# Performance work log

Measured on AMD Instinct MI355X. Metric: run time of the kernel, lower is better.

Reference implementation:

```python
import math
import jax, jax.numpy as jnp
import numpy as np

B, L, D, H = 4, 4096, 1024, 16
DK = D // H


def setup_inputs() -> dict:
    key = jax.random.key(0)
    ks = jax.random.split(key, 11)
    s = 0.02
    return {
        "queries": jax.random.normal(ks[0], (B, L, D), jnp.float32),
        "keys": jax.random.normal(ks[1], (B, L, D), jnp.float32),
        "values": jax.random.normal(ks[2], (B, L, D), jnp.float32),
        "Wq": jax.random.normal(ks[3], (D, D), jnp.float32) * s,
        "bq": jnp.zeros((D,), jnp.float32),
        "Wk": jax.random.normal(ks[4], (D, D), jnp.float32) * s,
        "bk": jnp.zeros((D,), jnp.float32),
        "Wv": jax.random.normal(ks[5], (D, D), jnp.float32) * s,
        "bv": jnp.zeros((D,), jnp.float32),
        "Wo": jax.random.normal(ks[6], (D, D), jnp.float32) * s,
        "bo": jnp.zeros((D,), jnp.float32),
    }


def reference(queries, keys, values, Wq, bq, Wk, bk, Wv, bv, Wo, bo):
    # projections + split heads: (B, H, L, DK)
    q = (queries @ Wq + bq).reshape(B, L, H, DK).transpose(0, 2, 1, 3)
    k = (keys @ Wk + bk).reshape(B, L, H, DK).transpose(0, 2, 1, 3)
    v = (values @ Wv + bv).reshape(B, L, H, DK).transpose(0, 2, 1, 3)

    # per-head mean over channel dim -> (B, H, L)
    qm = q.mean(axis=-1)
    km = k.mean(axis=-1)

    # FFT-based autocorrelation: corr (B, H, L)
    qf = jnp.fft.rfft(qm, axis=-1)
    kf = jnp.fft.rfft(km, axis=-1)
    corr = jnp.fft.irfft(qf * jnp.conj(kf), n=L, axis=-1)

    top_k = max(1, int(math.log(L)))  # top_k=None path -> 8 for L=4096
    w, delays = jax.lax.top_k(corr, top_k)          # (B, H, K)
    w = jax.nn.softmax(w, axis=-1)

    # torch.roll(x, shift=d): out[i] = x[(i - d) mod L]
    pos = jnp.arange(L)
    out = jnp.zeros_like(v)
    for kk in range(top_k):
        idx = (pos[None, None, :] - delays[:, :, kk, None]) % L  # (B, H, L)
        rolled = jnp.take_along_axis(v, idx[..., None], axis=2)  # (B, H, L, DK)
        out = out + w[:, :, kk, None, None] * rolled

    # merge heads (matches per-head concat order) and output projection
    out = out.transpose(0, 2, 1, 3).reshape(B, L, D)
    return out @ Wo + bo
```

## Files before the change

kernel.cpp:

```cpp
#include <hip/hip_runtime.h>
#include <hip/hip_bf16.h>
#include <cstdint>

#define BB 4
#define LL 4096
#define DD 1024
#define HH 16
#define DKH 64
#define MROWS 16384
#define KTOP 8
#define RPB 16

typedef float f32x4 __attribute__((ext_vector_type(4)));
typedef _Float16 f16;
typedef _Float16 f16x4 __attribute__((ext_vector_type(4)));
typedef _Float16 f16x8 __attribute__((ext_vector_type(8)));

__device__ __forceinline__ void gll16(const void* g, void* l) {
    __builtin_amdgcn_global_load_lds(
        (const __attribute__((address_space(1))) void*)g,
        (__attribute__((address_space(3))) void*)l, 16, 0, 0);
}

__global__ void k_colmeans(const float* __restrict__ Wq, const float* __restrict__ bq,
                           const float* __restrict__ Wk, const float* __restrict__ bk,
                           float* __restrict__ Wqm_t, float* __restrict__ Wkm_t,
                           float* __restrict__ bqm, float* __restrict__ bkm) {
    int t = blockIdx.x * blockDim.x + threadIdx.x;
    int which = t >> 14;
    int idx = t & 16383;
    int d = idx >> 4;
    int h = idx & 15;
    const float* W = which ? Wk : Wq;
    const float* p = W + d * DD + h * DKH;
    float s = 0.f;
    #pragma unroll
    for (int c = 0; c < DKH; ++c) s += p[c];
    (which ? Wkm_t : Wqm_t)[h * DD + d] = s * (1.0f / DKH);
    if (d == 0) {
        const float* bb = which ? bk : bq;
        float sb = 0.f;
        for (int c = 0; c < DKH; ++c) sb += bb[h * DKH + c];
        (which ? bkm : bqm)[h] = sb * (1.0f / DKH);
    }
}

__global__ void k_transpose_cvt(const float* __restrict__ in, f16* __restrict__ out) {
    __shared__ float tile[32][33];
    int k0 = blockIdx.x * 32;
    int n0 = blockIdx.y * 32;
    int tx = threadIdx.x, ty = threadIdx.y;
    #pragma unroll
    for (int j = 0; j < 32; j += 8)
        tile[ty + j][tx] = in[(k0 + ty + j) * DD + n0 + tx];
    __syncthreads();
    #pragma unroll
    for (int j = 0; j < 32; j += 8)
        out[(n0 + ty + j) * DD + k0 + tx] = (f16)tile[tx][ty + j];
}

__global__ void k_cvt_f16(const float* __restrict__ in, f16* __restrict__ out) {
    int i = blockIdx.x * blockDim.x + threadIdx.x;
    f32x4 v = ((const f32x4*)in)[i];
    f16x4 o;
    o[0] = (f16)v.x; o[1] = (f16)v.y; o[2] = (f16)v.z; o[3] = (f16)v.w;
    ((f16x4*)out)[i] = o;
}

__global__ __launch_bounds__(256, 4) void k_means(const float* __restrict__ q, const float* __restrict__ k,
                        const float* __restrict__ Wqm_t, const float* __restrict__ Wkm_t,
                        const float* __restrict__ bqm, const float* __restrict__ bkm,
                        float* __restrict__ qm, float* __restrict__ km) {
    __shared__ float lred[RPB * 64];
    int isK = blockIdx.x & 1;
    int rb  = blockIdx.x >> 1;
    const float* src = isK ? k : q;
    const float* W   = isK ? Wkm_t : Wqm_t;
    const float* bm  = isK ? bkm : bqm;
    float* dst = isK ? km : qm;
    int t = threadIdx.x;
    int wavei = t >> 6, lane = t & 63;
    int c = wavei * 256 + lane * 4;
    f32x4 wr[16];
    #pragma unroll
    for (int h = 0; h < 16; ++h) wr[h] = *(const f32x4*)(W + h * DD + c);
    const float* rbase = src + (size_t)rb * RPB * DD + c;
    #pragma unroll 2
    for (int r = 0; r < RPB; ++r) {
        f32x4 rv = *(const f32x4*)(rbase + r * DD);
        float v[16];
        #pragma unroll
        for (int h = 0; h < 16; ++h)
            v[h] = rv.x * wr[h].x + rv.y * wr[h].y + rv.z * wr[h].z + rv.w * wr[h].w;
        float u[8];
        #pragma unroll
        for (int i = 0; i < 8; ++i) {
            float keep = (lane & 1) ? v[2*i+1] : v[2*i];
            float send = (lane & 1) ? v[2*i]   : v[2*i+1];
            u[i] = keep + __shfl_xor(send, 1);
        }
        float w2[4];
        #pragma unroll
        for (int i = 0; i < 4; ++i) {
            float keep = (lane & 2) ? u[2*i+1] : u[2*i];
            float send = (lane & 2) ? u[2*i]   : u[2*i+1];
            w2[i] = keep + __shfl_xor(send, 2);
        }
        float y[2];
        #pragma unroll
        for (int i = 0; i < 2; ++i) {
            float keep = (lane & 4) ? w2[2*i+1] : w2[2*i];
            float send = (lane & 4) ? w2[2*i]   : w2[2*i+1];
            y[i] = keep + __shfl_xor(send, 4);
        }
        {
            float keep = (lane & 8) ? y[1] : y[0];
            float send = (lane & 8) ? y[0] : y[1];
            float z = keep + __shfl_xor(send, 8);
            z += __shfl_xor(z, 16);
            z += __shfl_xor(z, 32);
            if (lane < 16) lred[r * 64 + wavei * 16 + lane] = z;
        }
    }
    __syncthreads();
    int rr = t >> 4, h = t & 15;
    float s = lred[rr * 64 + h] + lred[rr * 64 + 16 + h]
            + lred[rr * 64 + 32 + h] + lred[rr * 64 + 48 + h] + bm[h];
    int row = rb * RPB + rr;
    int b = row >> 12, l = row & 4095;
    dst[((size_t)((b << 4) + h) << 12) + l] = s;
}

__global__ __launch_bounds__(1024) void k_corr(const float* __restrict__ qm,
                                               const float* __restrict__ km,
                                               float* __restrict__ corr) {
    __shared__ float sq[LL];
    __shared__ float sk[LL];
    __shared__ f32x4 red[1024];
    int bh = blockIdx.x >> 2;
    int lag0 = (blockIdx.x & 3) * 1024;
    const f32x4* qg = (const f32x4*)(qm + bh * LL);
    const f32x4* kg = (const f32x4*)(km + bh * LL);
    f32x4* sq4 = (f32x4*)sq;
    f32x4* sk4 = (f32x4*)sk;
    int t = threadIdx.x;
    for (int i = t; i < LL / 4; i += 1024) { sq4[i] = qg[i]; sk4[i] = kg[i]; }
    __syncthreads();
    int lt = t & 255;
    int ms = t >> 8;
    int d0 = lag0 + lt * 4;
    int m0 = ms * 1024;
    float a0 = 0, a1 = 0, a2 = 0, a3 = 0;
    f32x4 wv = sq4[((m0 + d0) & 4095) >> 2];
    float w0 = wv.x, w1 = wv.y, w2 = wv.z, w3 = wv.w;
    #pragma unroll 4
    for (int m = m0; m < m0 + 1024; m += 4) {
        f32x4 nx = sq4[((m + 4 + d0) & 4095) >> 2];
        f32x4 kv = sk4[m >> 2];
        a0 += kv.x * w0;  a1 += kv.x * w1;  a2 += kv.x * w2;  a3 += kv.x * w3;
        a0 += kv.y * w1;  a1 += kv.y * w2;  a2 += kv.y * w3;  a3 += kv.y * nx.x;
        a0 += kv.z * w2;  a1 += kv.z * w3;  a2 += kv.z * nx.x; a3 += kv.z * nx.y;
        a0 += kv.w * w3;  a1 += kv.w * nx.x; a2 += kv.w * nx.y; a3 += kv.w * nx.z;
        w0 = nx.x; w1 = nx.y; w2 = nx.z; w3 = nx.w;
    }
    f32x4 p; p.x = a0; p.y = a1; p.z = a2; p.w = a3;
    red[t] = p;
    __syncthreads();
    if (t < 256) {
        f32x4 s0 = red[t], s1 = red[256 + t], s2 = red[512 + t], s3 = red[768 + t];
        f32x4 s;
        s.x = s0.x + s1.x + s2.x + s3.x;
        s.y = s0.y + s1.y + s2.y + s3.y;
        s.z = s0.z + s1.z + s2.z + s3.z;
        s.w = s0.w + s1.w + s2.w + s3.w;
        *(f32x4*)(corr + bh * LL + lag0 + t * 4) = s;
    }
}

__global__ __launch_bounds__(256) void k_topk(const float* __restrict__ corr,
                                              float* __restrict__ wts, int* __restrict__ dls) {
    __shared__ float sc[LL];
    __shared__ float rv[4]; __shared__ int ri[4];
    __shared__ float topv[KTOP]; __shared__ int topi[KTOP];
    int bh = blockIdx.x;
    for (int i = threadIdx.x; i < LL; i += 256) sc[i] = corr[bh * LL + i];
    for (int kk = 0; kk < KTOP; ++kk) {
        __syncthreads();
        float bv = -1e30f; int bi = 0;
        for (int i = threadIdx.x; i < LL; i += 256) {
            float v = sc[i];
            if (v > bv) { bv = v; bi = i; }
        }
        #pragma unroll
        for (int off = 32; off; off >>= 1) {
            float ov = __shfl_down(bv, off);
            int oi = __shfl_down(bi, off);
            if (ov > bv || (ov == bv && oi < bi)) { bv = ov; bi = oi; }
        }
        int wid = threadIdx.x >> 6;
        if ((threadIdx.x & 63) == 0) { rv[wid] = bv; ri[wid] = bi; }
        __syncthreads();
        if (threadIdx.x == 0) {
            for (int w = 1; w < 4; ++w)
                if (rv[w] > bv || (rv[w] == bv && ri[w] < bi)) { bv = rv[w]; bi = ri[w]; }
            topv[kk] = bv; topi[kk] = bi;
            sc[bi] = -1e30f;
        }
    }
    __syncthreads();
    if (threadIdx.x == 0) {
        float mx = topv[0], s = 0.f, e[KTOP];
        #pragma unroll
        for (int kk = 0; kk < KTOP; ++kk) { e[kk] = __expf(topv[kk] - mx); s += e[kk]; }
        float inv = 1.0f / s;
        #pragma unroll
        for (int kk = 0; kk < KTOP; ++kk) {
            wts[bh * KTOP + kk] = e[kk] * inv;
            dls[bh * KTOP + kk] = topi[kk];
        }
    }
}

#define BM 128
#define BN 128
#define BKK 32
template <int MODE>
__global__ __launch_bounds__(256) void k_gemm_bt(const f16* __restrict__ A,
                                                 const f16* __restrict__ BT,
                                                 const float* __restrict__ bias,
                                                 void* __restrict__ Cout) {
    __shared__ f16 As[BM * BKK];
    __shared__ f16 Bs[BN * BKK];
    const int K = DD;
    int n0 = blockIdx.x * BN;
    int m0 = blockIdx.y * BM;
    int tid = threadIdx.x;
    int lane = tid & 63;
    int wave = tid >> 6;
    int wm = wave & 1, wn = wave >> 1;

    int row0 = tid >> 2;
    int slot = tid & 3;
    int kc0 = slot ^ ((row0 >> 1) & 3);
    int row1 = row0 + 64;
    int kc1 = slot ^ ((row1 >> 1) & 3);
    const f16* gA0 = A + (size_t)(m0 + row0) * K + kc0 * 8;
    const f16* gA1 = A + (size_t)(m0 + row1) * K + kc1 * 8;
    const f16* gB0 = BT + (size_t)(n0 + row0) * K + kc0 * 8;
    const f16* gB1 = BT + (size_t)(n0 + row1) * K + kc1 * 8;
    char* ldsA0 = (char*)As + wave * 1024;
    char* ldsA1 = (char*)As + 4096 + wave * 1024;
    char* ldsB0 = (char*)Bs + wave * 1024;
    char* ldsB1 = (char*)Bs + 4096 + wave * 1024;

    int fr = lane & 15;
    int quad = lane >> 4;
    int a_off[4], b_off[4];
    #pragma unroll
    for (int i = 0; i < 4; ++i) {
        int ra = wm * 64 + i * 16 + fr;
        a_off[i] = (ra * 4 + (quad ^ ((ra >> 1) & 3))) * 8;
        int rb = wn * 64 + i * 16 + fr;
        b_off[i] = (rb * 4 + (quad ^ ((rb >> 1) & 3))) * 8;
    }

    f32x4 acc[4][4] = {};
    for (int kt = 0; kt < K; kt += BKK) {
        __syncthreads();
        gll16(gA0, ldsA0);
        gll16(gA1, ldsA1);
        gll16(gB0, ldsB0);
        gll16(gB1, ldsB1);
        gA0 += BKK; gA1 += BKK; gB0 += BKK; gB1 += BKK;
        __syncthreads();
        f16x8 af[4], bf[4];
        #pragma unroll
        for (int i = 0; i < 4; ++i) af[i] = *(const f16x8*)(As + a_off[i]);
        #pragma unroll
        for (int i = 0; i < 4; ++i) bf[i] = *(const f16x8*)(Bs + b_off[i]);
        #pragma unroll
        for (int im = 0; im < 4; ++im)
            #pragma unroll
            for (int in = 0; in < 4; ++in)
                acc[im][in] = __builtin_amdgcn_mfma_f32_16x16x32_f16(af[im], bf[in], acc[im][in], 0, 0, 0);
    }

    #pragma unroll
    for (int in = 0; in < 4; ++in) {
        int col = n0 + wn * 64 + in * 16 + fr;
        float bb = bias[col];
        #pragma unroll
        for (int im = 0; im < 4; ++im) {
            int rowb = m0 + wm * 64 + im * 16 + quad * 4;
            #pragma unroll
            for (int r = 0; r < 4; ++r) {
                float val = acc[im][in][r] + bb;
                if (MODE == 0) {
                    int rr = rowb + r;
                    int b = rr >> 12, l = rr & 4095, h = col >> 6, c = col & 63;
                    ((f16*)Cout)[((size_t)(((b << 4) + h) << 12) + l) * 64 + c] = (f16)val;
                } else {
                    ((float*)Cout)[(size_t)(rowb + r) * DD + col] = val;
                }
            }
        }
    }
}

__global__ __launch_bounds__(256) void k_roll(const f16* __restrict__ V,
                                              const float* __restrict__ wts,
                                              const int* __restrict__ dls,
                                              f16* __restrict__ out) {
    int t = blockIdx.x * 256 + threadIdx.x;
    int cc = t & 7;
    int l = (t >> 3) & 4095;
    int bh = t >> 15;
    const f16* vb = V + ((size_t)bh << 18);
    float a[8] = {};
    #pragma unroll
    for (int kk = 0; kk < KTOP; ++kk) {
        float w = wts[bh * KTOP + kk];
        int d = dls[bh * KTOP + kk];
        int src = (l - d) & 4095;
        f16x8 vv = *(const f16x8*)(vb + (src << 6) + (cc << 3));
        #pragma unroll
        for (int j = 0; j < 8; ++j) a[j] += w * (float)vv[j];
    }
    f16* o = out + ((size_t)((bh >> 4) << 12) + l) * 1024 + ((bh & 15) << 6) + (cc << 3);
    f16x8 ov;
    #pragma unroll
    for (int j = 0; j < 8; ++j) ov[j] = (f16)a[j];
    *(f16x8*)o = ov;
}

extern "C" void kernel_launch(void* const* d_in, const int* in_sizes, int n_in,
                              void* d_out, int out_size, void* d_ws, size_t ws_size,
                              hipStream_t stream) {
    const float* queries = (const float*)d_in[0];
    const float* keys    = (const float*)d_in[1];
    const float* values  = (const float*)d_in[2];
    const float* Wq = (const float*)d_in[3];
    const float* bq = (const float*)d_in[4];
    const float* Wk = (const float*)d_in[5];
    const float* bk = (const float*)d_in[6];
    const float* Wv = (const float*)d_in[7];
    const float* bv = (const float*)d_in[8];
    const float* Wo = (const float*)d_in[9];
    const float* bo = (const float*)d_in[10];

    char* ws = (char*)d_ws;
    size_t off = 0;
    auto alloc = [&](size_t bytes) -> char* {
        char* p = ws + off;
        off += (bytes + 255) & ~(size_t)255;
        return p;
    };
    f16*   values_f16 = (f16*)alloc((size_t)MROWS * DD * 2);
    f16*   Vbuf       = (f16*)alloc((size_t)MROWS * DD * 2);
    f16*   WvT        = (f16*)alloc((size_t)DD * DD * 2);
    f16*   WoT        = (f16*)alloc((size_t)DD * DD * 2);
    float* Wqm_t      = (float*)alloc(HH * DD * 4);
    float* Wkm_t      = (float*)alloc(HH * DD * 4);
    float* bqm        = (float*)alloc(HH * 4);
    float* bkm        = (float*)alloc(HH * 4);
    float* qm         = (float*)alloc((size_t)BB * HH * LL * 4);
    float* km         = (float*)alloc((size_t)BB * HH * LL * 4);
    float* corr       = (float*)alloc((size_t)BB * HH * LL * 4);
    float* wts        = (float*)alloc(BB * HH * KTOP * 4);
    int*   dls        = (int*)alloc(BB * HH * KTOP * 4);
    f16*   out_f16    = values_f16;

    k_colmeans<<<128, 256, 0, stream>>>(Wq, bq, Wk, bk, Wqm_t, Wkm_t, bqm, bkm);
    k_transpose_cvt<<<dim3(32, 32), dim3(32, 8), 0, stream>>>(Wv, WvT);
    k_transpose_cvt<<<dim3(32, 32), dim3(32, 8), 0, stream>>>(Wo, WoT);
    k_cvt_f16<<<16384, 256, 0, stream>>>(values, values_f16);
    k_means<<<2048, 256, 0, stream>>>(queries, keys, Wqm_t, Wkm_t, bqm, bkm, qm, km);
    k_corr<<<256, 1024, 0, stream>>>(qm, km, corr);
    k_topk<<<64, 256, 0, stream>>>(corr, wts, dls);
    k_gemm_bt<0><<<dim3(DD / BN, MROWS / BM), 256, 0, stream>>>(values_f16, WvT, bv, Vbuf);
    k_roll<<<8192, 256, 0, stream>>>(Vbuf, wts, dls, out_f16);
    k_gemm_bt<1><<<dim3(DD / BN, MROWS / BM), 256, 0, stream>>>(out_f16, WoT, bo, d_out);
}
```

Measured before the change: 443.8 us.

## Use DPP reductions in means, drop LDS key copy in corr, swap GEMM grid order

In k_means, most cross-lane shuffles become DPP row operations, the next row is prefetched, and the final reduction moves partly into LDS with a larger, padded buffer. In k_corr, the key vector is no longer staged in LDS; it is read from global memory with a wave-uniform index so it can become a scalar/broadcast load. The GEMM grid is transposed so consecutive blocks walk along M rather than N, which changes which operand tiles are shared in L2. Together these aim to cut shuffle cost, LDS footprint and cache misses, at the risk of extra global traffic in k_corr and a different cache access pattern in the GEMMs.

```diff
diff --git a/kernel.cpp b/kernel.cpp
--- a/kernel.cpp
+++ b/kernel.cpp
@@ -20,6 +20,12 @@
     __builtin_amdgcn_global_load_lds(
         (const __attribute__((address_space(1))) void*)g,
         (__attribute__((address_space(3))) void*)l, 16, 0, 0);
+}
+
+template <int CTRL>
+__device__ __forceinline__ float dppf(float x) {
+    return __builtin_bit_cast(float,
+        __builtin_amdgcn_update_dpp(0, __builtin_bit_cast(int, x), CTRL, 0xF, 0xF, true));
 }
 
 __global__ void k_colmeans(const float* __restrict__ Wq, const float* __restrict__ bq,
@@ -71,7 +77,7 @@
                         const float* __restrict__ Wqm_t, const float* __restrict__ Wkm_t,
                         const float* __restrict__ bqm, const float* __restrict__ bkm,
                         float* __restrict__ qm, float* __restrict__ km) {
-    __shared__ float lred[RPB * 64];
+    __shared__ float lred[RPB * 264];
     int isK = blockIdx.x & 1;
     int rb  = blockIdx.x >> 1;
     const float* src = isK ? k : q;
@@ -84,10 +90,14 @@
     f32x4 wr[16];
     #pragma unroll
     for (int h = 0; h < 16; ++h) wr[h] = *(const f32x4*)(W + h * DD + c);
+    #pragma unroll
+    for (int h = 0; h < 16; ++h) asm volatile("" : "+v"(wr[h]));
     const float* rbase = src + (size_t)rb * RPB * DD + c;
-    #pragma unroll 2
+    f32x4 rv = *(const f32x4*)rbase;
+    #pragma unroll
     for (int r = 0; r < RPB; ++r) {
-        f32x4 rv = *(const f32x4*)(rbase + r * DD);
+        f32x4 nxt = rv;
+        if (r + 1 < RPB) nxt = *(const f32x4*)(rbase + (r + 1) * DD);
         float v[16];
         #pragma unroll
         for (int h = 0; h < 16; ++h)
@@ -97,35 +107,39 @@
         for (int i = 0; i < 8; ++i) {
             float keep = (lane & 1) ? v[2*i+1] : v[2*i];
             float send = (lane & 1) ? v[2*i]   : v[2*i+1];
-            u[i] = keep + __shfl_xor(send, 1);
+            u[i] = keep + dppf<0xB1>(send);
         }
         float w2[4];
         #pragma unroll
         for (int i = 0; i < 4; ++i) {
             float keep = (lane & 2) ? u[2*i+1] : u[2*i];
             float send = (lane & 2) ? u[2*i]   : u[2*i+1];
-            w2[i] = keep + __shfl_xor(send, 2);
+            w2[i] = keep + dppf<0x4E>(send);
         }
         float y[2];
         #pragma unroll
         for (int i = 0; i < 2; ++i) {
-            float keep = (lane & 4) ? w2[2*i+1] : w2[2*i];
-            float send = (lane & 4) ? w2[2*i]   : w2[2*i+1];
-            y[i] = keep + __shfl_xor(send, 4);
+            float keep = (lane & 8) ? w2[2*i+1] : w2[2*i];
+            float send = (lane & 8) ? w2[2*i]   : w2[2*i+1];
+            y[i] = keep + dppf<0x128>(send);
         }
         {
-            float keep = (lane & 8) ? y[1] : y[0];
-            float send = (lane & 8) ? y[0] : y[1];
-            float z = keep + __shfl_xor(send, 8);
-            z += __shfl_xor(z, 16);
-            z += __shfl_xor(z, 32);
-            if (lane < 16) lred[r * 64 + wavei * 16 + lane] = z;
-        }
+            float keep = (lane & 4) ? y[1] : y[0];
+            float send = (lane & 4) ? y[0] : y[1];
+            float z = keep + __shfl_xor(send, 4);
+            lred[r * 264 + wavei * 64 + lane] = z;
+        }
+        rv = nxt;
     }
     __syncthreads();
     int rr = t >> 4, h = t & 15;
-    float s = lred[rr * 64 + h] + lred[rr * 64 + 16 + h]
-            + lred[rr * 64 + 32 + h] + lred[rr * 64 + 48 + h] + bm[h];
+    int lp = (h & 3) | (((h >> 2) & 1) << 3) | (((h >> 3) & 1) << 2);
+    float s = bm[h];
+    #pragma unroll
+    for (int w = 0; w < 4; ++w)
+        #pragma unroll
+        for (int g = 0; g < 4; ++g)
+            s += lred[rr * 264 + w * 64 + g * 16 + lp];
     int row = rb * RPB + rr;
     int b = row >> 12, l = row & 4095;
     dst[((size_t)((b << 4) + h) << 12) + l] = s;
@@ -135,16 +149,14 @@
                                                const float* __restrict__ km,
                                                float* __restrict__ corr) {
     __shared__ float sq[LL];
-    __shared__ float sk[LL];
     __shared__ f32x4 red[1024];
     int bh = blockIdx.x >> 2;
     int lag0 = (blockIdx.x & 3) * 1024;
     const f32x4* qg = (const f32x4*)(qm + bh * LL);
     const f32x4* kg = (const f32x4*)(km + bh * LL);
     f32x4* sq4 = (f32x4*)sq;
-    f32x4* sk4 = (f32x4*)sk;
     int t = threadIdx.x;
-    for (int i = t; i < LL / 4; i += 1024) { sq4[i] = qg[i]; sk4[i] = kg[i]; }
+    for (int i = t; i < LL / 4; i += 1024) sq4[i] = qg[i];
     __syncthreads();
     int lt = t & 255;
     int ms = t >> 8;
@@ -156,7 +168,8 @@
     #pragma unroll 4
     for (int m = m0; m < m0 + 1024; m += 4) {
         f32x4 nx = sq4[((m + 4 + d0) & 4095) >> 2];
-        f32x4 kv = sk4[m >> 2];
+        int mi = __builtin_amdgcn_readfirstlane(m >> 2);
+        f32x4 kv = kg[mi];
         a0 += kv.x * w0;  a1 += kv.x * w1;  a2 += kv.x * w2;  a3 += kv.x * w3;
         a0 += kv.y * w1;  a1 += kv.y * w2;  a2 += kv.y * w3;  a3 += kv.y * nx.x;
         a0 += kv.z * w2;  a1 += kv.z * w3;  a2 += kv.z * nx.x; a3 += kv.z * nx.y;
@@ -232,8 +245,8 @@
     __shared__ f16 As[BM * BKK];
     __shared__ f16 Bs[BN * BKK];
     const int K = DD;
-    int n0 = blockIdx.x * BN;
-    int m0 = blockIdx.y * BM;
+    int m0 = blockIdx.x * BM;
+    int n0 = blockIdx.y * BN;
     int tid = threadIdx.x;
     int lane = tid & 63;
     int wave = tid >> 6;
@@ -377,7 +390,7 @@
     k_means<<<2048, 256, 0, stream>>>(queries, keys, Wqm_t, Wkm_t, bqm, bkm, qm, km);
     k_corr<<<256, 1024, 0, stream>>>(qm, km, corr);
     k_topk<<<64, 256, 0, stream>>>(corr, wts, dls);
-    k_gemm_bt<0><<<dim3(DD / BN, MROWS / BM), 256, 0, stream>>>(values_f16, WvT, bv, Vbuf);
+    k_gemm_bt<0><<<dim3(MROWS / BM, DD / BN), 256, 0, stream>>>(values_f16, WvT, bv, Vbuf);
     k_roll<<<8192, 256, 0, stream>>>(Vbuf, wts, dls, out_f16);
-    k_gemm_bt<1><<<dim3(DD / BN, MROWS / BM), 256, 0, stream>>>(out_f16, WoT, bo, d_out);
-}
+    k_gemm_bt<1><<<dim3(MROWS / BM, DD / BN), 256, 0, stream>>>(out_f16, WoT, bo, d_out);
+}
```

After: 443.8 us. No clear change (+0.0%).
